# Kernel optimization log

Hardware: AMD Instinct MI355X
Metric: run time of the kernel (lower is better)

The kernel has to match this reference:

```python
import jax, jax.numpy as jnp
import numpy as np

N_EXPERTS = 8
N_SHARED = 1
N_ROUTED = N_EXPERTS - N_SHARED          # 7
TOP_K_ROUTED = 3 - N_SHARED              # 2 routed experts per token
C = 1024
H = 4 * C


def _mlp(x, w_fc, w_proj):
    # x: [n, C]; w_fc: [C, H]; w_proj: [H, C]; exact (erf) GELU like torch nn.GELU
    return jax.nn.gelu(x @ w_fc, approximate=False) @ w_proj


def setup_inputs() -> dict:
    key = jax.random.key(0)
    ks = jax.random.split(key, 6)
    s = 0.02
    return {
        "x": jax.random.normal(ks[0], (4, 2048, C), dtype=jnp.float32),
        "gate_w": jax.random.normal(ks[1], (N_ROUTED, C), dtype=jnp.float32) * s,
        "lb_bias": jnp.zeros((N_ROUTED,), dtype=jnp.float32),
        "shared_wfc": jax.random.normal(ks[2], (C, H), dtype=jnp.float32) * s,
        "shared_wproj": jax.random.normal(ks[3], (H, C), dtype=jnp.float32) * s,
        "routed_wfc": jax.random.normal(ks[4], (N_ROUTED, C, H), dtype=jnp.float32) * s,
        "routed_wproj": jax.random.normal(ks[5], (N_ROUTED, H, C), dtype=jnp.float32) * s,
    }


def reference(x, gate_w, lb_bias, shared_wfc, shared_wproj, routed_wfc, routed_wproj):
    B, T, Cc = x.shape
    xt = x.reshape(-1, Cc)                       # [n, C]
    n = xt.shape[0]

    # shared expert(s) applied to every token
    shared_out = _mlp(xt, shared_wfc, shared_wproj)

    # routing
    routed_logits = xt @ gate_w.T                # [n, E_r]
    sel_logits = routed_logits + lb_bias
    _, topk_idx = jax.lax.top_k(sel_logits, TOP_K_ROUTED)   # [n, k]
    routed_probs = jax.nn.softmax(routed_logits.astype(jnp.float32), axis=-1)
    topk_w = jnp.take_along_axis(routed_probs, topk_idx, axis=-1)  # [n, k]

    # per-token combine weights over routed experts: [n, E_r]
    cw = jnp.zeros((n, N_ROUTED), dtype=jnp.float32)
    cw = cw.at[jnp.arange(n)[:, None], topk_idx].add(topk_w)

    # dispatch-combine: small fixed loop over routed experts
    routed_out = jnp.zeros_like(xt)
    for e in range(N_ROUTED):
        y = _mlp(xt, routed_wfc[e], routed_wproj[e])
        routed_out = routed_out + cw[:, e:e + 1] * y

    return (shared_out + routed_out).reshape(B, T, Cc)
```

## Files before the change

### kernel.cpp

```cpp
#include <hip/hip_runtime.h>
#include <hip/hip_bf16.h>

#define AS1 __attribute__((address_space(1)))
#define AS3 __attribute__((address_space(3)))

typedef __bf16 bf16x8 __attribute__((ext_vector_type(8)));
typedef float f32x4 __attribute__((ext_vector_type(4)));

static constexpr int C_DIM = 1024;
static constexpr int H_DIM = 4096;
static constexpr int NTOK  = 8192;
static constexpr int NR    = 7;
static constexpr int MAXG  = 17408;
static constexpr int MAXT  = 136;
static constexpr size_t WSZ = (size_t)C_DIM * H_DIM;

static __device__ __forceinline__ unsigned short f2bf(float f) {
  __hip_bfloat16 h = __float2bfloat16(f);
  return *reinterpret_cast<unsigned short*>(&h);
}

static __device__ __forceinline__ void gload16(const void* g, void* lds) {
  __builtin_amdgcn_global_load_lds((const AS1 void*)g, (AS3 void*)lds, 16, 0, 0);
}

__global__ __launch_bounds__(256) void cast_x_kernel(const float* __restrict__ x,
                                                     unsigned short* __restrict__ xb) {
  size_t i = ((size_t)blockIdx.x * blockDim.x + threadIdx.x) * 4;
  float4 v = *(const float4*)(x + i);
  ushort4 o;
  o.x = f2bf(v.x); o.y = f2bf(v.y); o.z = f2bf(v.z); o.w = f2bf(v.w);
  *(ushort4*)(xb + i) = o;
}

__global__ __launch_bounds__(256) void init_kernel(int* __restrict__ idx, int* __restrict__ cnt,
                                                   int* __restrict__ cursor) {
  int i = blockIdx.x * 256 + threadIdx.x;
  if (i < MAXG) idx[i] = 0;
  if (blockIdx.x == 0 && threadIdx.x < 8) { cnt[threadIdx.x] = 0; cursor[threadIdx.x] = 0; }
}

__global__ __launch_bounds__(256) void routing_kernel(const float* __restrict__ x,
                                                      const float* __restrict__ gw,
                                                      const float* __restrict__ bias,
                                                      float* __restrict__ cw,
                                                      int* __restrict__ cnt) {
  int wid = (int)((blockIdx.x * (size_t)blockDim.x + threadIdx.x) >> 6);
  int lane = threadIdx.x & 63;
  if (wid >= NTOK) return;
  const float* xt = x + (size_t)wid * C_DIM;
  float p[NR] = {0.f, 0.f, 0.f, 0.f, 0.f, 0.f, 0.f};
  for (int i = lane; i < C_DIM; i += 64) {
    float xv = xt[i];
#pragma unroll
    for (int e = 0; e < NR; ++e) p[e] += xv * gw[e * C_DIM + i];
  }
#pragma unroll
  for (int e = 0; e < NR; ++e) {
#pragma unroll
    for (int off = 32; off; off >>= 1) p[e] += __shfl_down(p[e], off);
  }
  if (lane == 0) {
    float m = p[0];
#pragma unroll
    for (int e = 1; e < NR; ++e) m = fmaxf(m, p[e]);
    float pr[NR], s = 0.f;
#pragma unroll
    for (int e = 0; e < NR; ++e) { pr[e] = __expf(p[e] - m); s += pr[e]; }
    float inv = 1.0f / s;
#pragma unroll
    for (int e = 0; e < NR; ++e) pr[e] *= inv;
    float sel[NR];
#pragma unroll
    for (int e = 0; e < NR; ++e) sel[e] = p[e] + bias[e];
    int i1 = 0;
#pragma unroll
    for (int e = 1; e < NR; ++e) if (sel[e] > sel[i1]) i1 = e;
    int i2 = -1;
#pragma unroll
    for (int e = 0; e < NR; ++e) {
      if (e == i1) continue;
      if (i2 < 0 || sel[e] > sel[i2]) i2 = e;
    }
    float c[NR] = {0.f, 0.f, 0.f, 0.f, 0.f, 0.f, 0.f};
    c[i1] = pr[i1];
    c[i2] += pr[i2];
#pragma unroll
    for (int e = 0; e < NR; ++e) cw[(size_t)wid * NR + e] = c[e];
    atomicAdd(&cnt[i1], 1);
    atomicAdd(&cnt[i2], 1);
  }
}

__global__ void scan_kernel(const int* __restrict__ cnt, int* __restrict__ offs,
                            int* __restrict__ tmap, int* __restrict__ ntiles) {
  int o = 0, nt = 0;
  for (int e = 0; e < NR; ++e) {
    offs[e] = o;
    int n = (cnt[e] + 127) & ~127;
    o += n;
    for (int tm = 0; tm < n; tm += 128) tmap[nt++] = (e << 16) | tm;
  }
  *ntiles = nt;
}

__global__ __launch_bounds__(256) void place_kernel(const float* __restrict__ cw,
                                                    const int* __restrict__ offs,
                                                    int* __restrict__ cursor,
                                                    int* __restrict__ idx,
                                                    int* __restrict__ tok2slot,
                                                    float* __restrict__ tok2w) {
  int t = blockIdx.x * 256 + threadIdx.x;
  if (t >= NTOK) return;
  int k = 0;
#pragma unroll
  for (int e = 0; e < NR; ++e) {
    float w = cw[(size_t)t * NR + e];
    if (w > 0.f) {
      int p = atomicAdd(&cursor[e], 1);
      int slot = offs[e] + p;
      idx[slot] = t;
      tok2slot[t * 2 + k] = slot;
      tok2w[t * 2 + k] = w;
      ++k;
    }
  }
}

__global__ void transpose_cast_all(const float* __restrict__ shared_w,
                                   const float* __restrict__ routed_w,
                                   unsigned short* __restrict__ out, int R, int S) {
  int e = blockIdx.z;
  const float* in = (e == 0) ? shared_w : routed_w + (size_t)(e - 1) * R * S;
  unsigned short* o = out + (size_t)e * R * S;
  __shared__ float t[32][33];
  int bx = blockIdx.x * 32;
  int by = blockIdx.y * 32;
  int tx = threadIdx.x, ty = threadIdx.y;
#pragma unroll
  for (int i = 0; i < 32; i += 8)
    t[ty + i][tx] = in[(size_t)(by + ty + i) * S + bx + tx];
  __syncthreads();
#pragma unroll
  for (int i = 0; i < 32; i += 8)
    o[(size_t)(bx + ty + i) * R + by + tx] = f2bf(t[tx][ty + i]);
}

template <bool GATHER>
__global__ __launch_bounds__(256) void gemm_fc(const unsigned short* __restrict__ A,
                                               const unsigned short* __restrict__ BtAll,
                                               unsigned short* __restrict__ Y,
                                               const int* __restrict__ idx,
                                               const int* __restrict__ offs,
                                               const int* __restrict__ tmap,
                                               const int* __restrict__ ntiles) {
  __shared__ __align__(16) unsigned short As[4 * 128 * 8];
  __shared__ __align__(16) unsigned short Bs[4 * 128 * 8];
  const int tid = threadIdx.x;
  const int wave = tid >> 6, lane = tid & 63;

  int m0, n0, base;
  const unsigned short* Bt;
  if (GATHER) {
    if (blockIdx.y >= *ntiles) return;
    const int packed = tmap[blockIdx.y];
    const int e = packed >> 16;
    m0 = packed & 0xffff;
    n0 = blockIdx.x * 128;
    base = offs[e];
    Bt = BtAll + (size_t)(e + 1) * WSZ;
  } else {
    const int f = blockIdx.y * gridDim.x + blockIdx.x;
    const int cpx = (gridDim.x * gridDim.y) >> 3;
    const int swz = (f & 7) * cpx + (f >> 3);
    m0 = (swz / gridDim.x) * 128;
    n0 = (swz % gridDim.x) * 128;
    base = 0;
    Bt = BtAll;
  }

  const int q0 = wave * 128 + lane, q1 = q0 + 64;
  const int kg0 = q0 >> 7, r0 = q0 & 127;
  const int kg1 = q1 >> 7, r1 = q1 & 127;
  const size_t rowA0 = GATHER ? (size_t)idx[base + m0 + r0] : (size_t)(m0 + r0);
  const size_t rowA1 = GATHER ? (size_t)idx[base + m0 + r1] : (size_t)(m0 + r1);
  const unsigned short* gA0 = A + rowA0 * C_DIM + kg0 * 8;
  const unsigned short* gA1 = A + rowA1 * C_DIM + kg1 * 8;
  const unsigned short* gB0 = Bt + (size_t)(n0 + r0) * C_DIM + kg0 * 8;
  const unsigned short* gB1 = Bt + (size_t)(n0 + r1) * C_DIM + kg1 * 8;
  unsigned short* lA0 = &As[(wave * 2 + 0) * 512];
  unsigned short* lA1 = &As[(wave * 2 + 1) * 512];
  unsigned short* lB0 = &Bs[(wave * 2 + 0) * 512];
  unsigned short* lB1 = &Bs[(wave * 2 + 1) * 512];

  const int wr = wave >> 1, wc = wave & 1;
  const int fr = lane & 15, fq = lane >> 4;
  f32x4 acc[4][4] = {};

  for (int k0 = 0; k0 < C_DIM; k0 += 32) {
    gload16(gA0 + k0, lA0);
    gload16(gA1 + k0, lA1);
    gload16(gB0 + k0, lB0);
    gload16(gB1 + k0, lB1);
    __syncthreads();
    bf16x8 af[4], bfr[4];
#pragma unroll
    for (int m = 0; m < 4; ++m)
      af[m] = *(const bf16x8*)&As[fq * 1024 + (wr * 64 + m * 16 + fr) * 8];
#pragma unroll
    for (int n = 0; n < 4; ++n)
      bfr[n] = *(const bf16x8*)&Bs[fq * 1024 + (wc * 64 + n * 16 + fr) * 8];
#pragma unroll
    for (int m = 0; m < 4; ++m)
#pragma unroll
      for (int n = 0; n < 4; ++n)
        acc[m][n] = __builtin_amdgcn_mfma_f32_16x16x32_bf16(af[m], bfr[n], acc[m][n], 0, 0, 0);
    __syncthreads();
  }

#pragma unroll
  for (int m = 0; m < 4; ++m)
#pragma unroll
    for (int n = 0; n < 4; ++n)
#pragma unroll
      for (int j = 0; j < 4; ++j) {
        const int row = m0 + wr * 64 + m * 16 + fq * 4 + j;
        const int col = n0 + wc * 64 + n * 16 + fr;
        const float v = acc[m][n][j];
        const float g = 0.5f * v * (1.0f + erff(v * 0.70710678118654752f));
        Y[(size_t)(base + row) * H_DIM + col] = f2bf(g);
      }
}

template <bool ROUTED>
__global__ __launch_bounds__(256) void gemm_proj(const unsigned short* __restrict__ Yg,
                                                 const unsigned short* __restrict__ BtAll,
                                                 float* __restrict__ Out,
                                                 const int* __restrict__ offs,
                                                 const int* __restrict__ tmap,
                                                 const int* __restrict__ ntiles) {
  __shared__ __align__(16) unsigned short As[4 * 128 * 8];
  __shared__ __align__(16) unsigned short Bs[4 * 128 * 8];
  const int tid = threadIdx.x;
  const int wave = tid >> 6, lane = tid & 63;

  int m0, n0, base;
  const unsigned short* Bt;
  if (ROUTED) {
    if (blockIdx.y >= *ntiles) return;
    const int packed = tmap[blockIdx.y];
    const int e = packed >> 16;
    m0 = packed & 0xffff;
    n0 = blockIdx.x * 128;
    base = offs[e];
    Bt = BtAll + (size_t)(e + 1) * WSZ;
  } else {
    const int f = blockIdx.y * gridDim.x + blockIdx.x;
    const int cpx = (gridDim.x * gridDim.y) >> 3;
    const int swz = (f & 7) * cpx + (f >> 3);
    m0 = (swz / gridDim.x) * 128;
    n0 = (swz % gridDim.x) * 128;
    base = 0;
    Bt = BtAll;
  }

  const int q0 = wave * 128 + lane, q1 = q0 + 64;
  const int kg0 = q0 >> 7, r0 = q0 & 127;
  const int kg1 = q1 >> 7, r1 = q1 & 127;
  const unsigned short* gA0 = Yg + (size_t)(base + m0 + r0) * H_DIM + kg0 * 8;
  const unsigned short* gA1 = Yg + (size_t)(base + m0 + r1) * H_DIM + kg1 * 8;
  const unsigned short* gB0 = Bt + (size_t)(n0 + r0) * H_DIM + kg0 * 8;
  const unsigned short* gB1 = Bt + (size_t)(n0 + r1) * H_DIM + kg1 * 8;
  unsigned short* lA0 = &As[(wave * 2 + 0) * 512];
  unsigned short* lA1 = &As[(wave * 2 + 1) * 512];
  unsigned short* lB0 = &Bs[(wave * 2 + 0) * 512];
  unsigned short* lB1 = &Bs[(wave * 2 + 1) * 512];

  const int wr = wave >> 1, wc = wave & 1;
  const int fr = lane & 15, fq = lane >> 4;
  f32x4 acc[4][4] = {};

  for (int k0 = 0; k0 < H_DIM; k0 += 32) {
    gload16(gA0 + k0, lA0);
    gload16(gA1 + k0, lA1);
    gload16(gB0 + k0, lB0);
    gload16(gB1 + k0, lB1);
    __syncthreads();
    bf16x8 af[4], bfr[4];
#pragma unroll
    for (int m = 0; m < 4; ++m)
      af[m] = *(const bf16x8*)&As[fq * 1024 + (wr * 64 + m * 16 + fr) * 8];
#pragma unroll
    for (int n = 0; n < 4; ++n)
      bfr[n] = *(const bf16x8*)&Bs[fq * 1024 + (wc * 64 + n * 16 + fr) * 8];
#pragma unroll
    for (int m = 0; m < 4; ++m)
#pragma unroll
      for (int n = 0; n < 4; ++n)
        acc[m][n] = __builtin_amdgcn_mfma_f32_16x16x32_bf16(af[m], bfr[n], acc[m][n], 0, 0, 0);
    __syncthreads();
  }

#pragma unroll
  for (int m = 0; m < 4; ++m)
#pragma unroll
    for (int n = 0; n < 4; ++n)
#pragma unroll
      for (int j = 0; j < 4; ++j) {
        const int p = wr * 64 + m * 16 + fq * 4 + j;
        const int col = n0 + wc * 64 + n * 16 + fr;
        const float v = acc[m][n][j];
        Out[(size_t)(base + m0 + p) * C_DIM + col] = v;
      }
}

__global__ __launch_bounds__(256) void combine_kernel(const float* __restrict__ Yout,
                                                      const int* __restrict__ tok2slot,
                                                      const float* __restrict__ tok2w,
                                                      float* __restrict__ out) {
  const int t = blockIdx.x;
  const int c4 = threadIdx.x;
  const int s0 = tok2slot[t * 2], s1 = tok2slot[t * 2 + 1];
  const float w0 = tok2w[t * 2], w1 = tok2w[t * 2 + 1];
  const float4 a = ((const float4*)(Yout + (size_t)s0 * C_DIM))[c4];
  const float4 b = ((const float4*)(Yout + (size_t)s1 * C_DIM))[c4];
  float4 o = ((float4*)(out + (size_t)t * C_DIM))[c4];
  o.x += w0 * a.x + w1 * b.x;
  o.y += w0 * a.y + w1 * b.y;
  o.z += w0 * a.z + w1 * b.z;
  o.w += w0 * a.w + w1 * b.w;
  ((float4*)(out + (size_t)t * C_DIM))[c4] = o;
}

extern "C" void kernel_launch(void* const* d_in, const int* in_sizes, int n_in,
                              void* d_out, int out_size, void* d_ws, size_t ws_size,
                              hipStream_t stream) {
  const float* x            = (const float*)d_in[0];
  const float* gate_w       = (const float*)d_in[1];
  const float* lb_bias      = (const float*)d_in[2];
  const float* shared_wfc   = (const float*)d_in[3];
  const float* shared_wproj = (const float*)d_in[4];
  const float* routed_wfc   = (const float*)d_in[5];
  const float* routed_wproj = (const float*)d_in[6];
  float* out = (float*)d_out;

  char* ws = (char*)d_ws;
  unsigned short* xb     = (unsigned short*)(ws);
  unsigned short* wfcT   = (unsigned short*)(ws + 16777216);
  float*          Yout   = (float*)(ws);
  unsigned short* wprojT = (unsigned short*)(ws + 83886080);
  unsigned short* Yg     = (unsigned short*)(ws + 150994944);
  float*          cw     = (float*)(ws + 293601280);
  int*            idx    = (int*)(ws + 293830656);
  int*            cnt    = (int*)(ws + 293900288);
  int*            offs   = (int*)(ws + 293900352);
  int*            cursor = (int*)(ws + 293900416);
  int*            tok2slot = (int*)(ws + 293900480);
  float*          tok2w    = (float*)(ws + 293966016);
  int*            tmap     = (int*)(ws + 294031552);
  int*            ntiles   = (int*)(ws + 294032128);

  cast_x_kernel<<<NTOK * C_DIM / (256 * 4), 256, 0, stream>>>(x, xb);
  init_kernel<<<(MAXG + 255) / 256, 256, 0, stream>>>(idx, cnt, cursor);
  routing_kernel<<<NTOK / 4, 256, 0, stream>>>(x, gate_w, lb_bias, cw, cnt);
  scan_kernel<<<1, 1, 0, stream>>>(cnt, offs, tmap, ntiles);
  place_kernel<<<NTOK / 256, 256, 0, stream>>>(cw, offs, cursor, idx, tok2slot, tok2w);

  transpose_cast_all<<<dim3(H_DIM / 32, C_DIM / 32, 8), dim3(32, 8), 0, stream>>>(
      shared_wfc, routed_wfc, wfcT, C_DIM, H_DIM);
  transpose_cast_all<<<dim3(C_DIM / 32, H_DIM / 32, 8), dim3(32, 8), 0, stream>>>(
      shared_wproj, routed_wproj, wprojT, H_DIM, C_DIM);

  gemm_fc<false><<<dim3(H_DIM / 128, NTOK / 128), 256, 0, stream>>>(
      xb, wfcT, Yg, idx, offs, tmap, ntiles);
  gemm_proj<false><<<dim3(C_DIM / 128, NTOK / 128), 256, 0, stream>>>(
      Yg, wprojT, out, offs, tmap, ntiles);

  gemm_fc<true><<<dim3(H_DIM / 128, MAXT), 256, 0, stream>>>(
      xb, wfcT, Yg, idx, offs, tmap, ntiles);
  gemm_proj<true><<<dim3(C_DIM / 128, MAXT), 256, 0, stream>>>(
      Yg, wprojT, Yout, offs, tmap, ntiles);

  combine_kernel<<<NTOK, 256, 0, stream>>>(Yout, tok2slot, tok2w, out);
}
```

Before: 1.342 ms.

## Double-buffer LDS tiles in fc and proj GEMMs to overlap loads with MFMA

Both GEMM kernels now keep two LDS buffers for the A and B tiles. The next K-slice is prefetched with global_load_lds into the alternate buffer while MFMAs run on the current one, and each iteration needs only one barrier instead of two. The aim is to hide global-memory latency behind matrix math. In exchange, LDS per block doubles, which may lower occupancy, and correctness depends on the barrier waiting for the outstanding async LDS loads.

```diff
diff --git a/kernel.cpp b/kernel.cpp
--- a/kernel.cpp
+++ b/kernel.cpp
@@ -154,8 +154,8 @@
                                                const int* __restrict__ offs,
                                                const int* __restrict__ tmap,
                                                const int* __restrict__ ntiles) {
-  __shared__ __align__(16) unsigned short As[4 * 128 * 8];
-  __shared__ __align__(16) unsigned short Bs[4 * 128 * 8];
+  __shared__ __align__(16) unsigned short As[2][4096];
+  __shared__ __align__(16) unsigned short Bs[2][4096];
   const int tid = threadIdx.x;
   const int wave = tid >> 6, lane = tid & 63;
 
@@ -188,34 +188,41 @@
   const unsigned short* gA1 = A + rowA1 * C_DIM + kg1 * 8;
   const unsigned short* gB0 = Bt + (size_t)(n0 + r0) * C_DIM + kg0 * 8;
   const unsigned short* gB1 = Bt + (size_t)(n0 + r1) * C_DIM + kg1 * 8;
-  unsigned short* lA0 = &As[(wave * 2 + 0) * 512];
-  unsigned short* lA1 = &As[(wave * 2 + 1) * 512];
-  unsigned short* lB0 = &Bs[(wave * 2 + 0) * 512];
-  unsigned short* lB1 = &Bs[(wave * 2 + 1) * 512];
+  const int c0 = (wave * 2 + 0) * 512, c1 = (wave * 2 + 1) * 512;
 
   const int wr = wave >> 1, wc = wave & 1;
   const int fr = lane & 15, fq = lane >> 4;
   f32x4 acc[4][4] = {};
 
+  gload16(gA0, &As[0][c0]);
+  gload16(gA1, &As[0][c1]);
+  gload16(gB0, &Bs[0][c0]);
+  gload16(gB1, &Bs[0][c1]);
+
+  int buf = 0;
   for (int k0 = 0; k0 < C_DIM; k0 += 32) {
-    gload16(gA0 + k0, lA0);
-    gload16(gA1 + k0, lA1);
-    gload16(gB0 + k0, lB0);
-    gload16(gB1 + k0, lB1);
     __syncthreads();
+    const int nk = k0 + 32;
+    if (nk < C_DIM) {
+      const int nb = buf ^ 1;
+      gload16(gA0 + nk, &As[nb][c0]);
+      gload16(gA1 + nk, &As[nb][c1]);
+      gload16(gB0 + nk, &Bs[nb][c0]);
+      gload16(gB1 + nk, &Bs[nb][c1]);
+    }
     bf16x8 af[4], bfr[4];
 #pragma unroll
     for (int m = 0; m < 4; ++m)
-      af[m] = *(const bf16x8*)&As[fq * 1024 + (wr * 64 + m * 16 + fr) * 8];
+      af[m] = *(const bf16x8*)&As[buf][fq * 1024 + (wr * 64 + m * 16 + fr) * 8];
 #pragma unroll
     for (int n = 0; n < 4; ++n)
-      bfr[n] = *(const bf16x8*)&Bs[fq * 1024 + (wc * 64 + n * 16 + fr) * 8];
+      bfr[n] = *(const bf16x8*)&Bs[buf][fq * 1024 + (wc * 64 + n * 16 + fr) * 8];
 #pragma unroll
     for (int m = 0; m < 4; ++m)
 #pragma unroll
       for (int n = 0; n < 4; ++n)
         acc[m][n] = __builtin_amdgcn_mfma_f32_16x16x32_bf16(af[m], bfr[n], acc[m][n], 0, 0, 0);
-    __syncthreads();
+    buf ^= 1;
   }
 
 #pragma unroll
@@ -239,8 +246,8 @@
                                                  const int* __restrict__ offs,
                                                  const int* __restrict__ tmap,
                                                  const int* __restrict__ ntiles) {
-  __shared__ __align__(16) unsigned short As[4 * 128 * 8];
-  __shared__ __align__(16) unsigned short Bs[4 * 128 * 8];
+  __shared__ __align__(16) unsigned short As[2][4096];
+  __shared__ __align__(16) unsigned short Bs[2][4096];
   const int tid = threadIdx.x;
   const int wave = tid >> 6, lane = tid & 63;
 
@@ -271,34 +278,41 @@
   const unsigned short* gA1 = Yg + (size_t)(base + m0 + r1) * H_DIM + kg1 * 8;
   const unsigned short* gB0 = Bt + (size_t)(n0 + r0) * H_DIM + kg0 * 8;
   const unsigned short* gB1 = Bt + (size_t)(n0 + r1) * H_DIM + kg1 * 8;
-  unsigned short* lA0 = &As[(wave * 2 + 0) * 512];
-  unsigned short* lA1 = &As[(wave * 2 + 1) * 512];
-  unsigned short* lB0 = &Bs[(wave * 2 + 0) * 512];
-  unsigned short* lB1 = &Bs[(wave * 2 + 1) * 512];
+  const int c0 = (wave * 2 + 0) * 512, c1 = (wave * 2 + 1) * 512;
 
   const int wr = wave >> 1, wc = wave & 1;
   const int fr = lane & 15, fq = lane >> 4;
   f32x4 acc[4][4] = {};
 
+  gload16(gA0, &As[0][c0]);
+  gload16(gA1, &As[0][c1]);
+  gload16(gB0, &Bs[0][c0]);
+  gload16(gB1, &Bs[0][c1]);
+
+  int buf = 0;
   for (int k0 = 0; k0 < H_DIM; k0 += 32) {
-    gload16(gA0 + k0, lA0);
-    gload16(gA1 + k0, lA1);
-    gload16(gB0 + k0, lB0);
-    gload16(gB1 + k0, lB1);
     __syncthreads();
+    const int nk = k0 + 32;
+    if (nk < H_DIM) {
+      const int nb = buf ^ 1;
+      gload16(gA0 + nk, &As[nb][c0]);
+      gload16(gA1 + nk, &As[nb][c1]);
+      gload16(gB0 + nk, &Bs[nb][c0]);
+      gload16(gB1 + nk, &Bs[nb][c1]);
+    }
     bf16x8 af[4], bfr[4];
 #pragma unroll
     for (int m = 0; m < 4; ++m)
-      af[m] = *(const bf16x8*)&As[fq * 1024 + (wr * 64 + m * 16 + fr) * 8];
+      af[m] = *(const bf16x8*)&As[buf][fq * 1024 + (wr * 64 + m * 16 + fr) * 8];
 #pragma unroll
     for (int n = 0; n < 4; ++n)
-      bfr[n] = *(const bf16x8*)&Bs[fq * 1024 + (wc * 64 + n * 16 + fr) * 8];
+      bfr[n] = *(const bf16x8*)&Bs[buf][fq * 1024 + (wc * 64 + n * 16 + fr) * 8];
 #pragma unroll
     for (int m = 0; m < 4; ++m)
 #pragma unroll
       for (int n = 0; n < 4; ++n)
         acc[m][n] = __builtin_amdgcn_mfma_f32_16x16x32_bf16(af[m], bfr[n], acc[m][n], 0, 0, 0);
-    __syncthreads();
+    buf ^= 1;
   }
 
 #pragma unroll
```

Result: no change. 1.338 ms (-0.3%).

## Triple-buffer LDS tiles with async prefetch two K-steps ahead in GEMMs

Applied to the files above, without the earlier changes.

Both the FC and projection GEMM kernels now keep three LDS buffers for the A and B tiles. Global-to-LDS loads are issued two K-iterations ahead, and explicit vmcnt waits let the current tile be consumed while later tiles are still in flight. This replaces the old load-then-sync-every-step pattern, whose global load latency was exposed each iteration. It triples LDS use per block, which may reduce occupancy, and it relies on hand-placed waitcnt and barrier ordering being correct.

```diff
diff --git a/kernel.cpp b/kernel.cpp
--- a/kernel.cpp
+++ b/kernel.cpp
@@ -146,6 +146,7 @@
     o[(size_t)(bx + ty + i) * R + by + tx] = f2bf(t[tx][ty + i]);
 }
 
+
 template <bool GATHER>
 __global__ __launch_bounds__(256) void gemm_fc(const unsigned short* __restrict__ A,
                                                const unsigned short* __restrict__ BtAll,
@@ -154,10 +155,11 @@
                                                const int* __restrict__ offs,
                                                const int* __restrict__ tmap,
                                                const int* __restrict__ ntiles) {
-  __shared__ __align__(16) unsigned short As[4 * 128 * 8];
-  __shared__ __align__(16) unsigned short Bs[4 * 128 * 8];
+  __shared__ __align__(16) unsigned short As[3][4096];
+  __shared__ __align__(16) unsigned short Bs[3][4096];
   const int tid = threadIdx.x;
   const int wave = tid >> 6, lane = tid & 63;
+  constexpr int NT = C_DIM / 32;
 
   int m0, n0, base;
   const unsigned short* Bt;
@@ -188,34 +190,46 @@
   const unsigned short* gA1 = A + rowA1 * C_DIM + kg1 * 8;
   const unsigned short* gB0 = Bt + (size_t)(n0 + r0) * C_DIM + kg0 * 8;
   const unsigned short* gB1 = Bt + (size_t)(n0 + r1) * C_DIM + kg1 * 8;
-  unsigned short* lA0 = &As[(wave * 2 + 0) * 512];
-  unsigned short* lA1 = &As[(wave * 2 + 1) * 512];
-  unsigned short* lB0 = &Bs[(wave * 2 + 0) * 512];
-  unsigned short* lB1 = &Bs[(wave * 2 + 1) * 512];
+  const int c0 = (wave * 2 + 0) * 512, c1 = (wave * 2 + 1) * 512;
 
   const int wr = wave >> 1, wc = wave & 1;
   const int fr = lane & 15, fq = lane >> 4;
   f32x4 acc[4][4] = {};
 
-  for (int k0 = 0; k0 < C_DIM; k0 += 32) {
-    gload16(gA0 + k0, lA0);
-    gload16(gA1 + k0, lA1);
-    gload16(gB0 + k0, lB0);
-    gload16(gB1 + k0, lB1);
-    __syncthreads();
+  asm volatile("s_waitcnt vmcnt(0)" ::: "memory");
+  gload16(gA0, &As[0][c0]); gload16(gA1, &As[0][c1]);
+  gload16(gB0, &Bs[0][c0]); gload16(gB1, &Bs[0][c1]);
+  gload16(gA0 + 32, &As[1][c0]); gload16(gA1 + 32, &As[1][c1]);
+  gload16(gB0 + 32, &Bs[1][c0]); gload16(gB1 + 32, &Bs[1][c1]);
+
+  int rb = 0;
+  for (int t = 0; t < NT; ++t) {
+    if (t + 2 < NT) {
+      const int wb = (rb >= 1) ? rb - 1 : rb + 2;
+      const int nk = (t + 2) * 32;
+      gload16(gA0 + nk, &As[wb][c0]); gload16(gA1 + nk, &As[wb][c1]);
+      gload16(gB0 + nk, &Bs[wb][c0]); gload16(gB1 + nk, &Bs[wb][c1]);
+      asm volatile("s_waitcnt vmcnt(8)" ::: "memory");
+    } else if (t + 1 < NT) {
+      asm volatile("s_waitcnt vmcnt(4)" ::: "memory");
+    } else {
+      asm volatile("s_waitcnt vmcnt(0)" ::: "memory");
+    }
+    __builtin_amdgcn_s_barrier();
     bf16x8 af[4], bfr[4];
 #pragma unroll
     for (int m = 0; m < 4; ++m)
-      af[m] = *(const bf16x8*)&As[fq * 1024 + (wr * 64 + m * 16 + fr) * 8];
+      af[m] = *(const bf16x8*)&As[rb][fq * 1024 + (wr * 64 + m * 16 + fr) * 8];
 #pragma unroll
     for (int n = 0; n < 4; ++n)
-      bfr[n] = *(const bf16x8*)&Bs[fq * 1024 + (wc * 64 + n * 16 + fr) * 8];
+      bfr[n] = *(const bf16x8*)&Bs[rb][fq * 1024 + (wc * 64 + n * 16 + fr) * 8];
 #pragma unroll
     for (int m = 0; m < 4; ++m)
 #pragma unroll
       for (int n = 0; n < 4; ++n)
         acc[m][n] = __builtin_amdgcn_mfma_f32_16x16x32_bf16(af[m], bfr[n], acc[m][n], 0, 0, 0);
-    __syncthreads();
+    __builtin_amdgcn_s_barrier();
+    rb = (rb == 2) ? 0 : rb + 1;
   }
 
 #pragma unroll
@@ -239,10 +253,11 @@
                                                  const int* __restrict__ offs,
                                                  const int* __restrict__ tmap,
                                                  const int* __restrict__ ntiles) {
-  __shared__ __align__(16) unsigned short As[4 * 128 * 8];
-  __shared__ __align__(16) unsigned short Bs[4 * 128 * 8];
+  __shared__ __align__(16) unsigned short As[3][4096];
+  __shared__ __align__(16) unsigned short Bs[3][4096];
   const int tid = threadIdx.x;
   const int wave = tid >> 6, lane = tid & 63;
+  constexpr int NT = H_DIM / 32;
 
   int m0, n0, base;
   const unsigned short* Bt;
@@ -271,34 +286,46 @@
   const unsigned short* gA1 = Yg + (size_t)(base + m0 + r1) * H_DIM + kg1 * 8;
   const unsigned short* gB0 = Bt + (size_t)(n0 + r0) * H_DIM + kg0 * 8;
   const unsigned short* gB1 = Bt + (size_t)(n0 + r1) * H_DIM + kg1 * 8;
-  unsigned short* lA0 = &As[(wave * 2 + 0) * 512];
-  unsigned short* lA1 = &As[(wave * 2 + 1) * 512];
-  unsigned short* lB0 = &Bs[(wave * 2 + 0) * 512];
-  unsigned short* lB1 = &Bs[(wave * 2 + 1) * 512];
+  const int c0 = (wave * 2 + 0) * 512, c1 = (wave * 2 + 1) * 512;
 
   const int wr = wave >> 1, wc = wave & 1;
   const int fr = lane & 15, fq = lane >> 4;
   f32x4 acc[4][4] = {};
 
-  for (int k0 = 0; k0 < H_DIM; k0 += 32) {
-    gload16(gA0 + k0, lA0);
-    gload16(gA1 + k0, lA1);
-    gload16(gB0 + k0, lB0);
-    gload16(gB1 + k0, lB1);
-    __syncthreads();
+  asm volatile("s_waitcnt vmcnt(0)" ::: "memory");
+  gload16(gA0, &As[0][c0]); gload16(gA1, &As[0][c1]);
+  gload16(gB0, &Bs[0][c0]); gload16(gB1, &Bs[0][c1]);
+  gload16(gA0 + 32, &As[1][c0]); gload16(gA1 + 32, &As[1][c1]);
+  gload16(gB0 + 32, &Bs[1][c0]); gload16(gB1 + 32, &Bs[1][c1]);
+
+  int rb = 0;
+  for (int t = 0; t < NT; ++t) {
+    if (t + 2 < NT) {
+      const int wb = (rb >= 1) ? rb - 1 : rb + 2;
+      const int nk = (t + 2) * 32;
+      gload16(gA0 + nk, &As[wb][c0]); gload16(gA1 + nk, &As[wb][c1]);
+      gload16(gB0 + nk, &Bs[wb][c0]); gload16(gB1 + nk, &Bs[wb][c1]);
+      asm volatile("s_waitcnt vmcnt(8)" ::: "memory");
+    } else if (t + 1 < NT) {
+      asm volatile("s_waitcnt vmcnt(4)" ::: "memory");
+    } else {
+      asm volatile("s_waitcnt vmcnt(0)" ::: "memory");
+    }
+    __builtin_amdgcn_s_barrier();
     bf16x8 af[4], bfr[4];
 #pragma unroll
     for (int m = 0; m < 4; ++m)
-      af[m] = *(const bf16x8*)&As[fq * 1024 + (wr * 64 + m * 16 + fr) * 8];
+      af[m] = *(const bf16x8*)&As[rb][fq * 1024 + (wr * 64 + m * 16 + fr) * 8];
 #pragma unroll
     for (int n = 0; n < 4; ++n)
-      bfr[n] = *(const bf16x8*)&Bs[fq * 1024 + (wc * 64 + n * 16 + fr) * 8];
+      bfr[n] = *(const bf16x8*)&Bs[rb][fq * 1024 + (wc * 64 + n * 16 + fr) * 8];
 #pragma unroll
     for (int m = 0; m < 4; ++m)
 #pragma unroll
       for (int n = 0; n < 4; ++n)
         acc[m][n] = __builtin_amdgcn_mfma_f32_16x16x32_bf16(af[m], bfr[n], acc[m][n], 0, 0, 0);
-    __syncthreads();
+    __builtin_amdgcn_s_barrier();
+    rb = (rb == 2) ? 0 : rb + 1;
   }
 
 #pragma unroll
```

New measurement: 1.282 ms. 1.05x faster.
